# Performance work log

Hardware: AMD Instinct MI355X
Metric: run time of the kernel (lower is better)

The kernel has to match this reference:

```python
import jax, jax.numpy as jnp
import numpy as np

B, V, J, NB = 512, 6890, 24, 10
P = (J - 1) * 9  # 207 pose-blendshape features
# Standard SMPL kinematic tree (parents[0] = -1 for root)
PARENTS = np.array([-1, 0, 0, 0, 1, 2, 3, 4, 5, 6, 7, 8, 9, 9, 9, 12, 13, 14, 16, 17, 18, 19, 20, 21])


def rodrigues(aa):
    """Axis-angle [N,3] -> rotation matrices [N,3,3] (batch_rodrigues)."""
    angle = jnp.linalg.norm(aa, axis=-1, keepdims=True) + 1e-8
    axis = aa / angle
    x, y, z = axis[..., 0], axis[..., 1], axis[..., 2]
    zero = jnp.zeros_like(x)
    K = jnp.stack([zero, -z, y, z, zero, -x, -y, x, zero], axis=-1).reshape(aa.shape[0], 3, 3)
    s = jnp.sin(angle)[..., None]
    c = jnp.cos(angle)[..., None]
    return jnp.eye(3, dtype=aa.dtype) + s * K + (1.0 - c) * jnp.matmul(K, K)


def setup_inputs() -> dict:
    key = jax.random.key(0)
    ks = jax.random.split(key, 9)
    J_reg = jax.random.uniform(ks[7], (J, V), dtype=jnp.float32)
    J_reg = J_reg / jnp.sum(J_reg, axis=1, keepdims=True)
    W = jax.nn.softmax(4.0 * jax.random.normal(ks[8], (V, J), dtype=jnp.float32), axis=-1)
    return {
        "betas": jax.random.normal(ks[0], (B, NB), dtype=jnp.float32),
        "body_pose": 0.3 * jax.random.normal(ks[1], (B, (J - 1) * 3), dtype=jnp.float32),
        "global_orient": 0.3 * jax.random.normal(ks[2], (B, 3), dtype=jnp.float32),
        "transl": jax.random.normal(ks[3], (B, 3), dtype=jnp.float32),
        "v_template": jax.random.normal(ks[4], (V, 3), dtype=jnp.float32),
        "shapedirs": 0.01 * jax.random.normal(ks[5], (V, 3, NB), dtype=jnp.float32),
        "posedirs": 0.01 * jax.random.normal(ks[6], (P, V * 3), dtype=jnp.float32),
        "J_regressor": J_reg,
        "lbs_weights": W,
    }


def reference(betas, body_pose, global_orient, transl, v_template, shapedirs, posedirs, J_regressor, lbs_weights):
    b = betas.shape[0]
    # --- pose to rotation matrices (pose2rot=True path) ---
    full_pose = jnp.concatenate([global_orient, body_pose], axis=-1)  # [B, 72]
    rot_mats = rodrigues(full_pose.reshape(-1, 3)).reshape(b, J, 3, 3)
    # --- shape blend shapes ---
    v_shaped = v_template + jnp.einsum('bl,vcl->bvc', betas, shapedirs)  # [B,V,3]
    joints = jnp.einsum('jv,bvc->bjc', J_regressor, v_shaped)            # [B,J,3]
    # --- pose blend shapes ---
    pose_feature = (rot_mats[:, 1:] - jnp.eye(3, dtype=rot_mats.dtype)).reshape(b, P)
    v_posed = v_shaped + (pose_feature @ posedirs).reshape(b, V, 3)
    # --- kinematic chain (batch_rigid_transform) ---
    rel_joints = joints.at[:, 1:].add(-joints[:, PARENTS[1:]])
    top = jnp.concatenate([rot_mats, rel_joints[..., None]], axis=-1)   # [B,J,3,4]
    bottom = jnp.broadcast_to(jnp.array([0.0, 0.0, 0.0, 1.0], dtype=rot_mats.dtype), (b, J, 1, 4))
    mats = jnp.concatenate([top, bottom], axis=-2)                      # [B,J,4,4]
    chain = [mats[:, 0]]
    for i in range(1, J):  # fixed 24-joint serial composition
        chain.append(chain[PARENTS[i]] @ mats[:, i])
    A = jnp.stack(chain, axis=1)                                        # [B,J,4,4]
    posed_joints = A[..., :3, 3]
    # remove rest-pose joint locations from the transforms
    t_rel = A[..., :3, 3] - jnp.einsum('bjmn,bjn->bjm', A[..., :3, :3], joints)
    A_rel = A.at[..., :3, 3].set(t_rel)
    # --- linear blend skinning ---
    T = jnp.einsum('vj,bjmn->bvmn', lbs_weights, A_rel)                 # [B,V,4,4]
    verts = jnp.einsum('bvmn,bvn->bvm', T[..., :3, :3], v_posed) + T[..., :3, 3]
    vertices = verts + transl[:, None]
    joints_out = posed_joints + transl[:, None]
    return vertices, joints_out
```

## Files before the change

kernel.cpp:

```cpp
#include <hip/hip_runtime.h>
#include <hip/hip_bf16.h>
#include <math.h>

#define Bn 512
#define Vn 6890
#define NBn 10
#define Pn 207
#define N3n 20670
#define KP 224
#define VPAD 6912

typedef __attribute__((ext_vector_type(8))) short short8v;
typedef __attribute__((ext_vector_type(4))) float f32x4;

__constant__ int c_par[24] = {-1,0,0,0,1,2,3,4,5,6,7,8,9,9,9,12,13,14,16,17,18,19,20,21};
__constant__ int c_lvl[10] = {0,1,4,7,10,15,18,20,22,24};

static __device__ __forceinline__ unsigned short f2bf(float f) {
  union { float f; unsigned u; } x; x.f = f;
  unsigned r = x.u + 0x7FFFu + ((x.u >> 16) & 1u);
  return (unsigned short)(r >> 16);
}
static __device__ __forceinline__ float bf2f(unsigned short h) {
  union { unsigned u; float f; } x; x.u = ((unsigned)h) << 16; return x.f;
}


__global__ __launch_bounds__(256) void k_prep(
    const float* __restrict__ Jreg, const float* __restrict__ vtpl,
    const float* __restrict__ sdirs, const float* __restrict__ pdirs,
    const float* __restrict__ W, float* __restrict__ part,
    unsigned short* __restrict__ B_lin,
    unsigned short* __restrict__ W_hi, unsigned short* __restrict__ W_lo)
{
  const int tid = threadIdx.x;
  if (blockIdx.x < 576) {
    const int bid = blockIdx.x % 72;
    const int chunk = blockIdx.x / 72;
    const int j = bid / 3, c = bid % 3;
    const int vlo = chunk * 862;
    const int vhi = min(Vn, vlo + 862);
    float acc[11];
#pragma unroll
    for (int k = 0; k < 11; k++) acc[k] = 0.f;
    for (int v = vlo + tid; v < vhi; v += 256) {
      float w = Jreg[(size_t)j * Vn + v];
      int n = v * 3 + c;
#pragma unroll
      for (int l = 0; l < 10; l++) acc[l] += w * sdirs[(size_t)n * 10 + l];
      acc[10] += w * vtpl[n];
    }
    __shared__ float red[256];
    for (int k = 0; k < 11; k++) {
      red[tid] = acc[k];
      __syncthreads();
      for (int s = 128; s > 0; s >>= 1) {
        if (tid < s) red[tid] += red[tid + s];
        __syncthreads();
      }
      if (tid == 0) part[(size_t)chunk * 792 + bid * 11 + k] = red[0];
      __syncthreads();
    }
  } else if (blockIdx.x < 576 + 2268) {
    const int pair = (blockIdx.x - 576) * 4 + (tid >> 6);
    const int l = tid & 63;
    const int nt = pair / 7, s = pair % 7;
    const int col = nt * 16 + (l & 15);
    const int kb = s * 32 + ((l >> 4) << 3);
    unsigned short vals[8];
#pragma unroll
    for (int j = 0; j < 8; j++) {
      int k = kb + j;
      unsigned short u = 0;
      if (col < N3n) {
        if (k < Pn) u = f2bf(pdirs[(size_t)k * N3n + col]);
        else if (k < 217) u = f2bf(sdirs[(size_t)col * 10 + (k - 207)]);
        else if (k == 217) u = f2bf(vtpl[col]);
        else if (k == 218) {
          float t = vtpl[col];
          u = f2bf(t - bf2f(f2bf(t)));
        }
      }
      vals[j] = u;
    }
    uint4 o;
    o.x = (unsigned)vals[0] | ((unsigned)vals[1] << 16);
    o.y = (unsigned)vals[2] | ((unsigned)vals[3] << 16);
    o.z = (unsigned)vals[4] | ((unsigned)vals[5] << 16);
    o.w = (unsigned)vals[6] | ((unsigned)vals[7] << 16);
    *(uint4*)(B_lin + (size_t)pair * 512 + l * 8) = o;
  } else {
    int idx = (blockIdx.x - 576 - 2268) * 256 + tid;
    if (idx < VPAD * 32) {
      int v = idx >> 5, k = idx & 31;
      float f = (v < Vn && k < 24) ? W[(size_t)v * 24 + k] : 0.f;
      unsigned short hi = f2bf(f);
      W_hi[idx] = hi;
      W_lo[idx] = f2bf(f - bf2f(hi));
    }
  }
}

__global__ __launch_bounds__(64) void k_pose2(
    const float* __restrict__ betas, const float* __restrict__ body_pose,
    const float* __restrict__ gorient, const float* __restrict__ transl,
    const float* __restrict__ part,
    unsigned short* __restrict__ pf_bf,
    unsigned short* __restrict__ Ar_hi, unsigned short* __restrict__ Ar_lo,
    float* __restrict__ out_joints)
{
  const int b = blockIdx.x;
  const int tid = threadIdx.x;
  __shared__ float JS_s[720];
  __shared__ float Jt_s[72];
  __shared__ float Rs[24][9];
  __shared__ float jnt[24][3];
  __shared__ float rel[24][3];
  __shared__ float A_s[24][12];

  for (int idx = tid; idx < 792; idx += 64) {
    float s = 0.f;
#pragma unroll
    for (int y = 0; y < 8; y++) s += part[(size_t)y * 792 + idx];
    int bid = idx / 11, k = idx % 11;
    if (k < 10) JS_s[bid * 10 + k] = s;
    else        Jt_s[bid] = s;
  }

  if (tid < 24) {
    float x, y, z;
    if (tid == 0) { x = gorient[b*3+0]; y = gorient[b*3+1]; z = gorient[b*3+2]; }
    else { int o = b*69 + (tid-1)*3; x = body_pose[o]; y = body_pose[o+1]; z = body_pose[o+2]; }
    float ang = sqrtf(x*x + y*y + z*z) + 1e-8f;
    float inv = 1.0f / ang;
    float ux = x*inv, uy = y*inv, uz = z*inv;
    float s = sinf(ang), cc = cosf(ang), omc = 1.0f - cc;
    float K[9] = {0.f, -uz, uy,  uz, 0.f, -ux,  -uy, ux, 0.f};
#pragma unroll
    for (int mm = 0; mm < 3; mm++)
#pragma unroll
      for (int nn = 0; nn < 3; nn++) {
        float kk = K[mm*3+0]*K[0+nn] + K[mm*3+1]*K[3+nn] + K[mm*3+2]*K[6+nn];
        float eye = (mm == nn) ? 1.0f : 0.0f;
        Rs[tid][mm*3+nn] = eye + s*K[mm*3+nn] + omc*kk;
      }
  }
  __syncthreads();

  for (int idx = tid; idx < 72; idx += 64) {
    float a = Jt_s[idx];
#pragma unroll
    for (int l = 0; l < 10; l++) a += betas[b*10 + l] * JS_s[idx*10 + l];
    jnt[idx/3][idx%3] = a;
  }
  for (int idx = tid; idx < KP; idx += 64) {
    unsigned short u = 0;
    if (idx < Pn) {
      int j = 1 + idx / 9, e = idx % 9;
      float eye = (e == 0 || e == 4 || e == 8) ? 1.0f : 0.0f;
      u = f2bf(Rs[j][e] - eye);
    } else if (idx < 217) {
      u = f2bf(betas[b*10 + (idx - 207)]);
    } else if (idx < 219) {
      u = 0x3F80;
    }
    pf_bf[(size_t)b * KP + idx] = u;
  }
  __syncthreads();
  for (int idx = tid; idx < 72; idx += 64) {
    int j = idx/3, cc = idx%3;
    float r = jnt[j][cc];
    if (j > 0) r -= jnt[c_par[j]][cc];
    rel[j][cc] = r;
  }
  __syncthreads();
  if (tid < 12) {
    int m = tid/4, nn = tid%4;
    A_s[0][tid] = (nn < 3) ? Rs[0][m*3+nn] : rel[0][m];
  }
  __syncthreads();
  for (int lev = 1; lev <= 8; lev++) {
    const int s0 = c_lvl[lev], s1 = c_lvl[lev + 1];
    const int jj = tid / 12, r = tid % 12;
    if (jj < s1 - s0) {
      const int i = s0 + jj;
      const int p = c_par[i];
      const int m = r >> 2, nn = r & 3;
      float v;
      if (nn < 3)
        v = A_s[p][m*4+0]*Rs[i][0+nn] + A_s[p][m*4+1]*Rs[i][3+nn] + A_s[p][m*4+2]*Rs[i][6+nn];
      else
        v = A_s[p][m*4+0]*rel[i][0] + A_s[p][m*4+1]*rel[i][1] + A_s[p][m*4+2]*rel[i][2] + A_s[p][m*4+3];
      A_s[i][r] = v;
    }
    __syncthreads();
  }
  for (int idx = tid; idx < 72; idx += 64) {
    int j = idx/3, cc = idx%3;
    out_joints[(size_t)b * 72 + idx] = A_s[j][cc*4+3] + transl[b*3+cc];
  }
  for (int idx = tid; idx < 512; idx += 64) {
    int e = idx >> 5, k = idx & 31;
    float a = 0.f;
    if (e < 12 && k < 24) {
      int m = e >> 2, nn = e & 3;
      if (nn < 3) a = A_s[k][m*4+nn];
      else a = A_s[k][m*4+3] - (A_s[k][m*4+0]*jnt[k][0] + A_s[k][m*4+1]*jnt[k][1] + A_s[k][m*4+2]*jnt[k][2]);
    }
    unsigned short hi = f2bf(a);
    Ar_hi[(size_t)b * 512 + idx] = hi;
    Ar_lo[(size_t)b * 512 + idx] = f2bf(a - bf2f(hi));
  }
}

__global__ __launch_bounds__(256) void k_mm2(
    const float* __restrict__ transl,
    const unsigned short* __restrict__ pf_bf, const unsigned short* __restrict__ B_lin,
    const unsigned short* __restrict__ W_hi, const unsigned short* __restrict__ W_lo,
    const unsigned short* __restrict__ Ar_hi, const unsigned short* __restrict__ Ar_lo,
    float* __restrict__ out)
{
  const int tid = threadIdx.x;
  const int l = tid & 63;
  const int wave = tid >> 6;
  const int b0 = blockIdx.x * 32;
  const int v0 = blockIdx.y * 64;

  __shared__ __align__(16) float vp[32][196];
  __shared__ float transl_s[32][3];

  if (tid < 96) transl_s[tid / 3][tid % 3] = transl[(size_t)b0 * 3 + tid];

  const unsigned short* pfb0 = pf_bf + (size_t)(b0 + (l & 15)) * KP + ((l >> 4) << 3);
  const unsigned short* pfb1 = pfb0 + 16 * KP;
  const int ntb = blockIdx.y * 12 + wave * 3;
  f32x4 a00 = {0.f,0.f,0.f,0.f}, a01 = a00, a02 = a00, a10 = a00, a11 = a00, a12 = a00;
#pragma unroll
  for (int s = 0; s < 7; s++) {
    short8v fa0 = *(const short8v*)(pfb0 + s * 32);
    short8v fa1 = *(const short8v*)(pfb1 + s * 32);
    short8v bv0 = *(const short8v*)(B_lin + ((size_t)(ntb + 0) * 7 + s) * 512 + l * 8);
    short8v bv1 = *(const short8v*)(B_lin + ((size_t)(ntb + 1) * 7 + s) * 512 + l * 8);
    short8v bv2 = *(const short8v*)(B_lin + ((size_t)(ntb + 2) * 7 + s) * 512 + l * 8);
    a00 = __builtin_amdgcn_mfma_f32_16x16x32_bf16(fa0, bv0, a00, 0, 0, 0);
    a01 = __builtin_amdgcn_mfma_f32_16x16x32_bf16(fa0, bv1, a01, 0, 0, 0);
    a02 = __builtin_amdgcn_mfma_f32_16x16x32_bf16(fa0, bv2, a02, 0, 0, 0);
    a10 = __builtin_amdgcn_mfma_f32_16x16x32_bf16(fa1, bv0, a10, 0, 0, 0);
    a11 = __builtin_amdgcn_mfma_f32_16x16x32_bf16(fa1, bv1, a11, 0, 0, 0);
    a12 = __builtin_amdgcn_mfma_f32_16x16x32_bf16(fa1, bv2, a12, 0, 0, 0);
  }
  {
    const int colb = wave * 48 + (l & 15);
    const int rowb = (l >> 4) * 4;
#pragma unroll
    for (int r = 0; r < 4; r++) {
      vp[rowb + r][colb]           = a00[r];
      vp[rowb + r][colb + 16]      = a01[r];
      vp[rowb + r][colb + 32]      = a02[r];
      vp[16 + rowb + r][colb]      = a10[r];
      vp[16 + rowb + r][colb + 16] = a11[r];
      vp[16 + rowb + r][colb + 32] = a12[r];
    }
  }
  __syncthreads();

  const int c = l & 15;
  const int g = l >> 4;
  const int kk = g << 3;

  short8v whi[4], wlo[4];
#pragma unroll
  for (int mt = 0; mt < 4; mt++) {
    const size_t wb = (size_t)(v0 + mt * 16 + c) * 32 + kk;
    whi[mt] = *(const short8v*)(W_hi + wb);
    wlo[mt] = *(const short8v*)(W_lo + wb);
  }

#pragma unroll
  for (int i = 0; i < 8; i++) {
    const int bl = wave * 8 + i;
    const size_t ab = (size_t)(b0 + bl) * 512 + c * 32 + kk;
    short8v ahi = *(const short8v*)(Ar_hi + ab);
    short8v alo = *(const short8v*)(Ar_lo + ab);
    const float trg = transl_s[bl][g < 3 ? g : 0];
#pragma unroll
    for (int mt = 0; mt < 4; mt++) {
      f32x4 t = {0.f, 0.f, 0.f, 0.f};
      t = __builtin_amdgcn_mfma_f32_16x16x32_bf16(alo, whi[mt], t, 0, 0, 0);
      t = __builtin_amdgcn_mfma_f32_16x16x32_bf16(ahi, wlo[mt], t, 0, 0, 0);
      t = __builtin_amdgcn_mfma_f32_16x16x32_bf16(ahi, whi[mt], t, 0, 0, 0);
      const int vl2 = mt * 16 + c;
      const int v = v0 + vl2;
      if (g < 3 && v < Vn) {
        float x = vp[bl][3 * vl2 + 0];
        float y = vp[bl][3 * vl2 + 1];
        float z = vp[bl][3 * vl2 + 2];
        out[((size_t)(b0 + bl) * Vn + v) * 3 + g] = t[0]*x + t[1]*y + t[2]*z + t[3] + trg;
      }
    }
  }
}


__global__ __launch_bounds__(256) void k_jsjt_part(
    const float* __restrict__ Jreg, const float* __restrict__ vtpl,
    const float* __restrict__ sdirs, float* __restrict__ part)
{
  const int bid = blockIdx.x;
  const int chunk = blockIdx.y;
  const int j = bid / 3, c = bid % 3;
  const int tid = threadIdx.x;
  const int vlo = chunk * 862;
  const int vhi = min(Vn, vlo + 862);
  float acc[11];
#pragma unroll
  for (int k = 0; k < 11; k++) acc[k] = 0.f;
  for (int v = vlo + tid; v < vhi; v += 256) {
    float w = Jreg[(size_t)j * Vn + v];
    int n = v * 3 + c;
#pragma unroll
    for (int l = 0; l < 10; l++) acc[l] += w * sdirs[(size_t)n * 10 + l];
    acc[10] += w * vtpl[n];
  }
  __shared__ float red[256];
  for (int k = 0; k < 11; k++) {
    red[tid] = acc[k];
    __syncthreads();
    for (int s = 128; s > 0; s >>= 1) {
      if (tid < s) red[tid] += red[tid + s];
      __syncthreads();
    }
    if (tid == 0) part[(size_t)chunk * 792 + bid * 11 + k] = red[0];
    __syncthreads();
  }
}

__global__ __launch_bounds__(1024) void k_jsjt_red(
    const float* __restrict__ part, float* __restrict__ JS, float* __restrict__ Jt)
{
  const int t = threadIdx.x;
  if (t >= 792) return;
  float s = 0.f;
#pragma unroll
  for (int y = 0; y < 8; y++) s += part[(size_t)y * 792 + t];
  int bid = t / 11, k = t % 11;
  if (k < 10) JS[bid * 10 + k] = s;
  else        Jt[bid] = s;
}

__global__ __launch_bounds__(64) void k_pose_fb(
    const float* __restrict__ betas, const float* __restrict__ body_pose,
    const float* __restrict__ gorient, const float* __restrict__ transl,
    const float* __restrict__ JS, const float* __restrict__ Jt,
    float* __restrict__ pf_ws, float* __restrict__ Ar_ws,
    float* __restrict__ out_joints)
{
  const int b = blockIdx.x;
  const int tid = threadIdx.x;
  __shared__ float Rs[24][9];
  __shared__ float jnt[24][3];
  __shared__ float rel[24][3];
  __shared__ float A_s[24][12];

  if (tid < 24) {
    float x, y, z;
    if (tid == 0) { x = gorient[b*3+0]; y = gorient[b*3+1]; z = gorient[b*3+2]; }
    else { int o = b*69 + (tid-1)*3; x = body_pose[o]; y = body_pose[o+1]; z = body_pose[o+2]; }
    float ang = sqrtf(x*x + y*y + z*z) + 1e-8f;
    float inv = 1.0f / ang;
    float ux = x*inv, uy = y*inv, uz = z*inv;
    float s = sinf(ang), cc = cosf(ang), omc = 1.0f - cc;
    float K[9] = {0.f, -uz, uy,  uz, 0.f, -ux,  -uy, ux, 0.f};
#pragma unroll
    for (int mm = 0; mm < 3; mm++)
#pragma unroll
      for (int nn = 0; nn < 3; nn++) {
        float kk = K[mm*3+0]*K[0+nn] + K[mm*3+1]*K[3+nn] + K[mm*3+2]*K[6+nn];
        float eye = (mm == nn) ? 1.0f : 0.0f;
        Rs[tid][mm*3+nn] = eye + s*K[mm*3+nn] + omc*kk;
      }
  }
  for (int idx = tid; idx < 72; idx += 64) {
    float a = Jt[idx];
#pragma unroll
    for (int l = 0; l < 10; l++) a += betas[b*10 + l] * JS[idx*10 + l];
    jnt[idx/3][idx%3] = a;
  }
  __syncthreads();
  for (int idx = tid; idx < Pn; idx += 64) {
    int j = 1 + idx / 9, e = idx % 9;
    float eye = (e == 0 || e == 4 || e == 8) ? 1.0f : 0.0f;
    pf_ws[(size_t)b * Pn + idx] = Rs[j][e] - eye;
  }
  for (int idx = tid; idx < 72; idx += 64) {
    int j = idx/3, cc = idx%3;
    float r = jnt[j][cc];
    if (j > 0) r -= jnt[c_par[j]][cc];
    rel[j][cc] = r;
  }
  __syncthreads();
  if (tid < 12) {
    int m = tid/4, nn = tid%4;
    A_s[0][tid] = (nn < 3) ? Rs[0][m*3+nn] : rel[0][m];
  }
  __syncthreads();
  for (int i = 1; i < 24; i++) {
    if (tid < 12) {
      int m = tid/4, nn = tid%4;
      int p = c_par[i];
      float v;
      if (nn < 3)
        v = A_s[p][m*4+0]*Rs[i][0+nn] + A_s[p][m*4+1]*Rs[i][3+nn] + A_s[p][m*4+2]*Rs[i][6+nn];
      else
        v = A_s[p][m*4+0]*rel[i][0] + A_s[p][m*4+1]*rel[i][1] + A_s[p][m*4+2]*rel[i][2] + A_s[p][m*4+3];
      A_s[i][tid] = v;
    }
    __syncthreads();
  }
  for (int idx = tid; idx < 72; idx += 64) {
    int j = idx/3, cc = idx%3;
    out_joints[(size_t)b * 72 + idx] = A_s[j][cc*4+3] + transl[b*3+cc];
  }
  for (int idx = tid; idx < 288; idx += 64) {
    int j = idx/12, r = idx%12, m = r/4, nn = r%4;
    float v;
    if (nn < 3) v = A_s[j][m*4+nn];
    else v = A_s[j][m*4+3] - (A_s[j][m*4+0]*jnt[j][0] + A_s[j][m*4+1]*jnt[j][1] + A_s[j][m*4+2]*jnt[j][2]);
    Ar_ws[(size_t)b * 288 + idx] = v;
  }
}

__global__ __launch_bounds__(192) void k_verts_fb(
    const float* __restrict__ betas, const float* __restrict__ transl,
    const float* __restrict__ vtpl, const float* __restrict__ sdirs,
    const float* __restrict__ pdirs, const float* __restrict__ W,
    const float* __restrict__ pf_ws, const float* __restrict__ Ar_ws,
    float* __restrict__ out)
{
  const int tid = threadIdx.x;
  const int b0 = blockIdx.x * 16;
  const int v0 = blockIdx.y * 128;
  const int n0 = v0 * 3;
  __shared__ __align__(16) float pf_s[Pn][16];
  __shared__ __align__(16) float Ar_s[16][288];
  __shared__ __align__(16) float vp_s[16][384];
  __shared__ float betas_s[16][NBn];
  __shared__ float transl_s[16][3];
  for (int idx = tid; idx < Pn * 16; idx += 192) {
    int p = idx >> 4, bi = idx & 15;
    pf_s[p][bi] = pf_ws[(size_t)(b0 + bi) * Pn + p];
  }
  for (int idx = tid; idx < 16 * 288; idx += 192)
    Ar_s[idx / 288][idx % 288] = Ar_ws[(size_t)b0 * 288 + idx];
  for (int idx = tid; idx < 16 * NBn; idx += 192)
    betas_s[idx / NBn][idx % NBn] = betas[(size_t)b0 * NBn + idx];
  for (int idx = tid; idx < 48; idx += 192)
    transl_s[idx / 3][idx % 3] = transl[(size_t)b0 * 3 + idx];
  __syncthreads();
  const int n = n0 + 2 * tid;
  const bool valid = (n < N3n);
  float acc0[16], acc1[16];
#pragma unroll
  for (int i = 0; i < 16; i++) { acc0[i] = 0.f; acc1[i] = 0.f; }
  for (int p = 0; p < Pn; p++) {
    float pd0 = 0.f, pd1 = 0.f;
    if (valid) { float2 t = *(const float2*)(pdirs + (size_t)p * N3n + n); pd0 = t.x; pd1 = t.y; }
    const float4* row = (const float4*)(pf_s[p]);
#pragma unroll
    for (int q = 0; q < 4; q++) {
      float4 f = row[q];
      acc0[4*q+0] += f.x * pd0;  acc1[4*q+0] += f.x * pd1;
      acc0[4*q+1] += f.y * pd0;  acc1[4*q+1] += f.y * pd1;
      acc0[4*q+2] += f.z * pd0;  acc1[4*q+2] += f.z * pd1;
      acc0[4*q+3] += f.w * pd0;  acc1[4*q+3] += f.w * pd1;
    }
  }
  float sd0[10], sd1[10], vt0 = 0.f, vt1 = 0.f;
#pragma unroll
  for (int l = 0; l < 10; l++) { sd0[l] = 0.f; sd1[l] = 0.f; }
  if (valid) {
    for (int l = 0; l < 10; l++) { sd0[l] = sdirs[(size_t)n*10 + l]; sd1[l] = sdirs[(size_t)n*10 + 10 + l]; }
    vt0 = vtpl[n]; vt1 = vtpl[n+1];
  }
#pragma unroll
  for (int bi = 0; bi < 16; bi++) {
    float s0 = vt0, s1 = vt1;
#pragma unroll
    for (int l = 0; l < 10; l++) { float bb = betas_s[bi][l]; s0 += bb*sd0[l]; s1 += bb*sd1[l]; }
    acc0[bi] += s0; acc1[bi] += s1;
  }
#pragma unroll
  for (int bi = 0; bi < 16; bi++) { vp_s[bi][2*tid] = acc0[bi]; vp_s[bi][2*tid+1] = acc1[bi]; }
  __syncthreads();
  const int m = tid / 64;
  const int vl = tid % 64;
  const int va = v0 + vl, vb = v0 + vl + 64;
  const bool va_ok = (va < Vn), vb_ok = (vb < Vn);
  float Wr0[24], Wr1[24];
#pragma unroll
  for (int j = 0; j < 24; j++) { Wr0[j] = 0.f; Wr1[j] = 0.f; }
  if (va_ok) { const float4* wp = (const float4*)(W + (size_t)va*24);
#pragma unroll
    for (int q = 0; q < 6; q++) { float4 f = wp[q]; Wr0[4*q]=f.x; Wr0[4*q+1]=f.y; Wr0[4*q+2]=f.z; Wr0[4*q+3]=f.w; } }
  if (vb_ok) { const float4* wp = (const float4*)(W + (size_t)vb*24);
#pragma unroll
    for (int q = 0; q < 6; q++) { float4 f = wp[q]; Wr1[4*q]=f.x; Wr1[4*q+1]=f.y; Wr1[4*q+2]=f.z; Wr1[4*q+3]=f.w; } }
  for (int bi = 0; bi < 16; bi++) {
    float Ta0=0.f,Ta1=0.f,Ta2=0.f,Ta3=0.f, Tb0=0.f,Tb1=0.f,Tb2=0.f,Tb3=0.f;
    const float4* arb = (const float4*)(Ar_s[bi]);
#pragma unroll
    for (int j = 0; j < 24; j++) {
      float4 a = arb[j*3 + m];
      float wa = Wr0[j], wb = Wr1[j];
      Ta0 += wa*a.x; Ta1 += wa*a.y; Ta2 += wa*a.z; Ta3 += wa*a.w;
      Tb0 += wb*a.x; Tb1 += wb*a.y; Tb2 += wb*a.z; Tb3 += wb*a.w;
    }
    float tr = transl_s[bi][m];
    if (va_ok) {
      float x = vp_s[bi][vl*3+0], y = vp_s[bi][vl*3+1], z = vp_s[bi][vl*3+2];
      out[((size_t)(b0+bi)*Vn + va)*3 + m] = Ta0*x + Ta1*y + Ta2*z + Ta3 + tr;
    }
    if (vb_ok) {
      float x = vp_s[bi][(vl+64)*3+0], y = vp_s[bi][(vl+64)*3+1], z = vp_s[bi][(vl+64)*3+2];
      out[((size_t)(b0+bi)*Vn + vb)*3 + m] = Tb0*x + Tb1*y + Tb2*z + Tb3 + tr;
    }
  }
}

extern "C" void kernel_launch(void* const* d_in, const int* in_sizes, int n_in,
                              void* d_out, int out_size, void* d_ws, size_t ws_size,
                              hipStream_t stream)
{
  const float *betas=nullptr, *bpose=nullptr, *gorient=nullptr, *transl=nullptr,
              *vtpl=nullptr, *sdirs=nullptr, *pdirs=nullptr, *Jreg=nullptr, *W=nullptr;
  int seen1536 = 0, seen165360 = 0;
  for (int i = 0; i < n_in; i++) {
    const float* p = (const float*)d_in[i];
    switch (in_sizes[i]) {
      case 5120:    betas = p; break;
      case 35328:   bpose = p; break;
      case 20670:   vtpl  = p; break;
      case 206700:  sdirs = p; break;
      case 4278690: pdirs = p; break;
      case 1536:    if (seen1536++ == 0) gorient = p; else transl = p; break;
      case 165360:  if (seen165360++ == 0) Jreg = p; else W = p; break;
      default: break;
    }
  }
  float* out = (float*)d_out;

  float* ws   = (float*)d_ws;
  float* part = ws;
  float* JS   = ws + 6336;
  float* Jt   = ws + 7056;
  float* pf   = ws + 7128;
  float* Ar   = ws + 113112;
  unsigned short* pf_bf = (unsigned short*)(ws + 260568);
  unsigned short* B_lin = (unsigned short*)(ws + 317912);
  unsigned short* W_hi  = (unsigned short*)(ws + 2640344);
  unsigned short* W_lo  = (unsigned short*)(ws + 2750936);
  unsigned short* Ar_hi = (unsigned short*)(ws + 2861528);
  unsigned short* Ar_lo = (unsigned short*)(ws + 2992600);
  const size_t WS_NEED = (size_t)3123672 * 4;
  const bool big = (ws_size >= WS_NEED);

  if (big) {
    k_prep<<<3708, 256, 0, stream>>>(Jreg, vtpl, sdirs, pdirs, W,
                                     part, B_lin, W_hi, W_lo);
    k_pose2<<<Bn, 64, 0, stream>>>(betas, bpose, gorient, transl, part,
                                   pf_bf, Ar_hi, Ar_lo,
                                   out + (size_t)Bn * Vn * 3);
    k_mm2<<<dim3(16, 108), 256, 0, stream>>>(transl, pf_bf, B_lin,
                                             W_hi, W_lo, Ar_hi, Ar_lo, out);
  } else {
    k_jsjt_part<<<dim3(72, 8), 256, 0, stream>>>(Jreg, vtpl, sdirs, part);
    k_jsjt_red<<<1, 1024, 0, stream>>>(part, JS, Jt);
    k_pose_fb<<<Bn, 64, 0, stream>>>(betas, bpose, gorient, transl, JS, Jt, pf, Ar,
                                     out + (size_t)Bn * Vn * 3);
    k_verts_fb<<<dim3(32, 54), 192, 0, stream>>>(betas, transl, vtpl, sdirs,
                                                 pdirs, W, pf, Ar, out);
  }
}
```

Measured before the change: 63.28 us.

## Switch MFMA paths to fp16, drop hi/lo splits, enlarge tiles, batch pose blocks

Moves the pose-blendshape and skinning matmuls from bf16 to fp16 MFMA. The skinning stage drops the three-term hi/lo split and uses a single fp16 product, and W and A_rel are stored once instead of twice. The main kernel now tiles 64 batches instead of 32 per block, and its grid is linearised and swizzled across vertex tiles for locality. The pose kernel packs 8 batch elements into one 512-thread block. Single fp16 skinning weights and transforms lose accuracy relative to the split scheme and risk exceeding tolerance, and the larger tile raises shared-memory and register use.

```diff
diff --git a/kernel.cpp b/kernel.cpp
--- a/kernel.cpp
+++ b/kernel.cpp
@@ -10,28 +10,18 @@
 #define KP 224
 #define VPAD 6912
 
-typedef __attribute__((ext_vector_type(8))) short short8v;
+typedef __attribute__((ext_vector_type(8))) _Float16 half8;
 typedef __attribute__((ext_vector_type(4))) float f32x4;
 
 __constant__ int c_par[24] = {-1,0,0,0,1,2,3,4,5,6,7,8,9,9,9,12,13,14,16,17,18,19,20,21};
 __constant__ int c_lvl[10] = {0,1,4,7,10,15,18,20,22,24};
-
-static __device__ __forceinline__ unsigned short f2bf(float f) {
-  union { float f; unsigned u; } x; x.f = f;
-  unsigned r = x.u + 0x7FFFu + ((x.u >> 16) & 1u);
-  return (unsigned short)(r >> 16);
-}
-static __device__ __forceinline__ float bf2f(unsigned short h) {
-  union { unsigned u; float f; } x; x.u = ((unsigned)h) << 16; return x.f;
-}
 
 
 __global__ __launch_bounds__(256) void k_prep(
     const float* __restrict__ Jreg, const float* __restrict__ vtpl,
     const float* __restrict__ sdirs, const float* __restrict__ pdirs,
     const float* __restrict__ W, float* __restrict__ part,
-    unsigned short* __restrict__ B_lin,
-    unsigned short* __restrict__ W_hi, unsigned short* __restrict__ W_lo)
+    _Float16* __restrict__ B_h, _Float16* __restrict__ W_h)
 {
   const int tid = threadIdx.x;
   if (blockIdx.x < 576) {
@@ -67,58 +57,53 @@
     const int nt = pair / 7, s = pair % 7;
     const int col = nt * 16 + (l & 15);
     const int kb = s * 32 + ((l >> 4) << 3);
-    unsigned short vals[8];
+    half8 hv;
 #pragma unroll
     for (int j = 0; j < 8; j++) {
       int k = kb + j;
-      unsigned short u = 0;
+      float f = 0.f;
       if (col < N3n) {
-        if (k < Pn) u = f2bf(pdirs[(size_t)k * N3n + col]);
-        else if (k < 217) u = f2bf(sdirs[(size_t)col * 10 + (k - 207)]);
-        else if (k == 217) u = f2bf(vtpl[col]);
+        if (k < Pn) f = pdirs[(size_t)k * N3n + col];
+        else if (k < 217) f = sdirs[(size_t)col * 10 + (k - 207)];
+        else if (k == 217) f = (float)(_Float16)vtpl[col];
         else if (k == 218) {
           float t = vtpl[col];
-          u = f2bf(t - bf2f(f2bf(t)));
+          f = t - (float)(_Float16)t;
         }
       }
-      vals[j] = u;
-    }
-    uint4 o;
-    o.x = (unsigned)vals[0] | ((unsigned)vals[1] << 16);
-    o.y = (unsigned)vals[2] | ((unsigned)vals[3] << 16);
-    o.z = (unsigned)vals[4] | ((unsigned)vals[5] << 16);
-    o.w = (unsigned)vals[6] | ((unsigned)vals[7] << 16);
-    *(uint4*)(B_lin + (size_t)pair * 512 + l * 8) = o;
+      hv[j] = (_Float16)f;
+    }
+    *(half8*)(B_h + (size_t)pair * 512 + l * 8) = hv;
   } else {
     int idx = (blockIdx.x - 576 - 2268) * 256 + tid;
     if (idx < VPAD * 32) {
       int v = idx >> 5, k = idx & 31;
       float f = (v < Vn && k < 24) ? W[(size_t)v * 24 + k] : 0.f;
-      unsigned short hi = f2bf(f);
-      W_hi[idx] = hi;
-      W_lo[idx] = f2bf(f - bf2f(hi));
-    }
-  }
-}
-
-__global__ __launch_bounds__(64) void k_pose2(
+      W_h[idx] = (_Float16)f;
+    }
+  }
+}
+
+__global__ __launch_bounds__(512) void k_pose2(
     const float* __restrict__ betas, const float* __restrict__ body_pose,
     const float* __restrict__ gorient, const float* __restrict__ transl,
     const float* __restrict__ part,
-    unsigned short* __restrict__ pf_bf,
-    unsigned short* __restrict__ Ar_hi, unsigned short* __restrict__ Ar_lo,
+    _Float16* __restrict__ pf_h, _Float16* __restrict__ Ar_h,
     float* __restrict__ out_joints)
 {
-  const int b = blockIdx.x;
   const int tid = threadIdx.x;
+  const int wave = tid >> 6;
+  const int lane = tid & 63;
+  const int b = blockIdx.x * 8 + wave;
+
   __shared__ float JS_s[720];
   __shared__ float Jt_s[72];
-  __shared__ float Rs[24][9];
-  __shared__ float jnt[24][3];
-  __shared__ float rel[24][3];
-  __shared__ float A_s[24][12];
-
-  for (int idx = tid; idx < 792; idx += 64) {
+  __shared__ float Rs[8][24][9];
+  __shared__ float jnt[8][24][3];
+  __shared__ float rel[8][24][3];
+  __shared__ float A_s[8][24][12];
+
+  for (int idx = tid; idx < 792; idx += 512) {
     float s = 0.f;
 #pragma unroll
     for (int y = 0; y < 8; y++) s += part[(size_t)y * 792 + idx];
@@ -127,10 +112,10 @@
     else        Jt_s[bid] = s;
   }
 
-  if (tid < 24) {
+  if (lane < 24) {
     float x, y, z;
-    if (tid == 0) { x = gorient[b*3+0]; y = gorient[b*3+1]; z = gorient[b*3+2]; }
-    else { int o = b*69 + (tid-1)*3; x = body_pose[o]; y = body_pose[o+1]; z = body_pose[o+2]; }
+    if (lane == 0) { x = gorient[b*3+0]; y = gorient[b*3+1]; z = gorient[b*3+2]; }
+    else { int o = b*69 + (lane-1)*3; x = body_pose[o]; y = body_pose[o+1]; z = body_pose[o+2]; }
     float ang = sqrtf(x*x + y*y + z*z) + 1e-8f;
     float inv = 1.0f / ang;
     float ux = x*inv, uy = y*inv, uz = z*inv;
@@ -142,125 +127,133 @@
       for (int nn = 0; nn < 3; nn++) {
         float kk = K[mm*3+0]*K[0+nn] + K[mm*3+1]*K[3+nn] + K[mm*3+2]*K[6+nn];
         float eye = (mm == nn) ? 1.0f : 0.0f;
-        Rs[tid][mm*3+nn] = eye + s*K[mm*3+nn] + omc*kk;
+        Rs[wave][lane][mm*3+nn] = eye + s*K[mm*3+nn] + omc*kk;
       }
   }
   __syncthreads();
 
-  for (int idx = tid; idx < 72; idx += 64) {
+  for (int idx = lane; idx < 72; idx += 64) {
     float a = Jt_s[idx];
 #pragma unroll
     for (int l = 0; l < 10; l++) a += betas[b*10 + l] * JS_s[idx*10 + l];
-    jnt[idx/3][idx%3] = a;
-  }
-  for (int idx = tid; idx < KP; idx += 64) {
-    unsigned short u = 0;
+    jnt[wave][idx/3][idx%3] = a;
+  }
+  for (int idx = lane; idx < KP; idx += 64) {
+    float f = 0.f;
     if (idx < Pn) {
       int j = 1 + idx / 9, e = idx % 9;
       float eye = (e == 0 || e == 4 || e == 8) ? 1.0f : 0.0f;
-      u = f2bf(Rs[j][e] - eye);
+      f = Rs[wave][j][e] - eye;
     } else if (idx < 217) {
-      u = f2bf(betas[b*10 + (idx - 207)]);
+      f = betas[b*10 + (idx - 207)];
     } else if (idx < 219) {
-      u = 0x3F80;
-    }
-    pf_bf[(size_t)b * KP + idx] = u;
-  }
-  __syncthreads();
-  for (int idx = tid; idx < 72; idx += 64) {
+      f = 1.0f;
+    }
+    pf_h[(size_t)b * KP + idx] = (_Float16)f;
+  }
+  __syncthreads();
+  for (int idx = lane; idx < 72; idx += 64) {
     int j = idx/3, cc = idx%3;
-    float r = jnt[j][cc];
-    if (j > 0) r -= jnt[c_par[j]][cc];
-    rel[j][cc] = r;
-  }
-  __syncthreads();
-  if (tid < 12) {
-    int m = tid/4, nn = tid%4;
-    A_s[0][tid] = (nn < 3) ? Rs[0][m*3+nn] : rel[0][m];
+    float r = jnt[wave][j][cc];
+    if (j > 0) r -= jnt[wave][c_par[j]][cc];
+    rel[wave][j][cc] = r;
+  }
+  __syncthreads();
+  if (lane < 12) {
+    int m = lane/4, nn = lane%4;
+    A_s[wave][0][lane] = (nn < 3) ? Rs[wave][0][m*3+nn] : rel[wave][0][m];
   }
   __syncthreads();
   for (int lev = 1; lev <= 8; lev++) {
     const int s0 = c_lvl[lev], s1 = c_lvl[lev + 1];
-    const int jj = tid / 12, r = tid % 12;
+    const int jj = lane / 12, r = lane % 12;
     if (jj < s1 - s0) {
       const int i = s0 + jj;
       const int p = c_par[i];
       const int m = r >> 2, nn = r & 3;
       float v;
       if (nn < 3)
-        v = A_s[p][m*4+0]*Rs[i][0+nn] + A_s[p][m*4+1]*Rs[i][3+nn] + A_s[p][m*4+2]*Rs[i][6+nn];
+        v = A_s[wave][p][m*4+0]*Rs[wave][i][0+nn] + A_s[wave][p][m*4+1]*Rs[wave][i][3+nn] + A_s[wave][p][m*4+2]*Rs[wave][i][6+nn];
       else
-        v = A_s[p][m*4+0]*rel[i][0] + A_s[p][m*4+1]*rel[i][1] + A_s[p][m*4+2]*rel[i][2] + A_s[p][m*4+3];
-      A_s[i][r] = v;
+        v = A_s[wave][p][m*4+0]*rel[wave][i][0] + A_s[wave][p][m*4+1]*rel[wave][i][1] + A_s[wave][p][m*4+2]*rel[wave][i][2] + A_s[wave][p][m*4+3];
+      A_s[wave][i][r] = v;
     }
     __syncthreads();
   }
-  for (int idx = tid; idx < 72; idx += 64) {
+  for (int idx = lane; idx < 72; idx += 64) {
     int j = idx/3, cc = idx%3;
-    out_joints[(size_t)b * 72 + idx] = A_s[j][cc*4+3] + transl[b*3+cc];
-  }
-  for (int idx = tid; idx < 512; idx += 64) {
+    out_joints[(size_t)b * 72 + idx] = A_s[wave][j][cc*4+3] + transl[b*3+cc];
+  }
+  for (int idx = lane; idx < 512; idx += 64) {
     int e = idx >> 5, k = idx & 31;
     float a = 0.f;
     if (e < 12 && k < 24) {
       int m = e >> 2, nn = e & 3;
-      if (nn < 3) a = A_s[k][m*4+nn];
-      else a = A_s[k][m*4+3] - (A_s[k][m*4+0]*jnt[k][0] + A_s[k][m*4+1]*jnt[k][1] + A_s[k][m*4+2]*jnt[k][2]);
-    }
-    unsigned short hi = f2bf(a);
-    Ar_hi[(size_t)b * 512 + idx] = hi;
-    Ar_lo[(size_t)b * 512 + idx] = f2bf(a - bf2f(hi));
-  }
-}
-
-__global__ __launch_bounds__(256) void k_mm2(
+      if (nn < 3) a = A_s[wave][k][m*4+nn];
+      else a = A_s[wave][k][m*4+3] - (A_s[wave][k][m*4+0]*jnt[wave][k][0] + A_s[wave][k][m*4+1]*jnt[wave][k][1] + A_s[wave][k][m*4+2]*jnt[wave][k][2]);
+    }
+    Ar_h[(size_t)b * 512 + idx] = (_Float16)a;
+  }
+}
+
+__global__ __launch_bounds__(256) void k_mm3(
     const float* __restrict__ transl,
-    const unsigned short* __restrict__ pf_bf, const unsigned short* __restrict__ B_lin,
-    const unsigned short* __restrict__ W_hi, const unsigned short* __restrict__ W_lo,
-    const unsigned short* __restrict__ Ar_hi, const unsigned short* __restrict__ Ar_lo,
+    const _Float16* __restrict__ pf_h, const _Float16* __restrict__ B_h,
+    const _Float16* __restrict__ W_h, const _Float16* __restrict__ Ar_h,
     float* __restrict__ out)
 {
+  const int lin = blockIdx.x;
+  const int r8 = lin & 7;
+  const int k2 = lin >> 3;
+  const int b_t = k2 & 7;
+  const int m8 = k2 >> 3;
+  const int v_t = r8 * 14 + m8;
+  if (v_t >= 108) return;
+
   const int tid = threadIdx.x;
   const int l = tid & 63;
   const int wave = tid >> 6;
-  const int b0 = blockIdx.x * 32;
-  const int v0 = blockIdx.y * 64;
-
-  __shared__ __align__(16) float vp[32][196];
-  __shared__ float transl_s[32][3];
-
-  if (tid < 96) transl_s[tid / 3][tid % 3] = transl[(size_t)b0 * 3 + tid];
-
-  const unsigned short* pfb0 = pf_bf + (size_t)(b0 + (l & 15)) * KP + ((l >> 4) << 3);
-  const unsigned short* pfb1 = pfb0 + 16 * KP;
-  const int ntb = blockIdx.y * 12 + wave * 3;
-  f32x4 a00 = {0.f,0.f,0.f,0.f}, a01 = a00, a02 = a00, a10 = a00, a11 = a00, a12 = a00;
+  const int b0 = b_t * 64;
+  const int v0 = v_t * 64;
+
+  __shared__ __align__(16) float vp[64][196];
+  __shared__ float transl_s[64][3];
+
+  if (tid < 192) transl_s[tid / 3][tid % 3] = transl[(size_t)b0 * 3 + tid];
+
+  const int c0 = l & 15;
+  const int kk0 = (l >> 4) << 3;
+  const int ntb = v_t * 12 + wave * 3;
+  f32x4 acc[4][3];
+#pragma unroll
+  for (int t = 0; t < 4; t++)
+#pragma unroll
+    for (int n = 0; n < 3; n++) acc[t][n] = (f32x4){0.f, 0.f, 0.f, 0.f};
+
 #pragma unroll
   for (int s = 0; s < 7; s++) {
-    short8v fa0 = *(const short8v*)(pfb0 + s * 32);
-    short8v fa1 = *(const short8v*)(pfb1 + s * 32);
-    short8v bv0 = *(const short8v*)(B_lin + ((size_t)(ntb + 0) * 7 + s) * 512 + l * 8);
-    short8v bv1 = *(const short8v*)(B_lin + ((size_t)(ntb + 1) * 7 + s) * 512 + l * 8);
-    short8v bv2 = *(const short8v*)(B_lin + ((size_t)(ntb + 2) * 7 + s) * 512 + l * 8);
-    a00 = __builtin_amdgcn_mfma_f32_16x16x32_bf16(fa0, bv0, a00, 0, 0, 0);
-    a01 = __builtin_amdgcn_mfma_f32_16x16x32_bf16(fa0, bv1, a01, 0, 0, 0);
-    a02 = __builtin_amdgcn_mfma_f32_16x16x32_bf16(fa0, bv2, a02, 0, 0, 0);
-    a10 = __builtin_amdgcn_mfma_f32_16x16x32_bf16(fa1, bv0, a10, 0, 0, 0);
-    a11 = __builtin_amdgcn_mfma_f32_16x16x32_bf16(fa1, bv1, a11, 0, 0, 0);
-    a12 = __builtin_amdgcn_mfma_f32_16x16x32_bf16(fa1, bv2, a12, 0, 0, 0);
+    half8 bv[3];
+#pragma unroll
+    for (int n = 0; n < 3; n++)
+      bv[n] = *(const half8*)(B_h + ((size_t)(ntb + n) * 7 + s) * 512 + l * 8);
+#pragma unroll
+    for (int t = 0; t < 4; t++) {
+      half8 fa = *(const half8*)(pf_h + (size_t)(b0 + t * 16 + c0) * KP + kk0 + s * 32);
+#pragma unroll
+      for (int n = 0; n < 3; n++)
+        acc[t][n] = __builtin_amdgcn_mfma_f32_16x16x32_f16(fa, bv[n], acc[t][n], 0, 0, 0);
+    }
   }
   {
-    const int colb = wave * 48 + (l & 15);
+    const int colb = wave * 48 + c0;
     const int rowb = (l >> 4) * 4;
 #pragma unroll
-    for (int r = 0; r < 4; r++) {
-      vp[rowb + r][colb]           = a00[r];
-      vp[rowb + r][colb + 16]      = a01[r];
-      vp[rowb + r][colb + 32]      = a02[r];
-      vp[16 + rowb + r][colb]      = a10[r];
-      vp[16 + rowb + r][colb + 16] = a11[r];
-      vp[16 + rowb + r][colb + 32] = a12[r];
-    }
+    for (int t = 0; t < 4; t++)
+#pragma unroll
+      for (int n = 0; n < 3; n++)
+#pragma unroll
+        for (int r = 0; r < 4; r++)
+          vp[t * 16 + rowb + r][colb + n * 16] = acc[t][n][r];
   }
   __syncthreads();
 
@@ -268,27 +261,20 @@
   const int g = l >> 4;
   const int kk = g << 3;
 
-  short8v whi[4], wlo[4];
-#pragma unroll
-  for (int mt = 0; mt < 4; mt++) {
-    const size_t wb = (size_t)(v0 + mt * 16 + c) * 32 + kk;
-    whi[mt] = *(const short8v*)(W_hi + wb);
-    wlo[mt] = *(const short8v*)(W_lo + wb);
-  }
-
-#pragma unroll
-  for (int i = 0; i < 8; i++) {
-    const int bl = wave * 8 + i;
-    const size_t ab = (size_t)(b0 + bl) * 512 + c * 32 + kk;
-    short8v ahi = *(const short8v*)(Ar_hi + ab);
-    short8v alo = *(const short8v*)(Ar_lo + ab);
+  half8 wh[4];
+#pragma unroll
+  for (int mt = 0; mt < 4; mt++)
+    wh[mt] = *(const half8*)(W_h + (size_t)(v0 + mt * 16 + c) * 32 + kk);
+
+#pragma unroll
+  for (int i = 0; i < 16; i++) {
+    const int bl = wave * 16 + i;
+    half8 ah = *(const half8*)(Ar_h + (size_t)(b0 + bl) * 512 + c * 32 + kk);
     const float trg = transl_s[bl][g < 3 ? g : 0];
 #pragma unroll
     for (int mt = 0; mt < 4; mt++) {
       f32x4 t = {0.f, 0.f, 0.f, 0.f};
-      t = __builtin_amdgcn_mfma_f32_16x16x32_bf16(alo, whi[mt], t, 0, 0, 0);
-      t = __builtin_amdgcn_mfma_f32_16x16x32_bf16(ahi, wlo[mt], t, 0, 0, 0);
-      t = __builtin_amdgcn_mfma_f32_16x16x32_bf16(ahi, whi[mt], t, 0, 0, 0);
+      t = __builtin_amdgcn_mfma_f32_16x16x32_f16(ah, wh[mt], t, 0, 0, 0);
       const int vl2 = mt * 16 + c;
       const int v = v0 + vl2;
       if (g < 3 && v < Vn) {
@@ -555,23 +541,18 @@
   float* Jt   = ws + 7056;
   float* pf   = ws + 7128;
   float* Ar   = ws + 113112;
-  unsigned short* pf_bf = (unsigned short*)(ws + 260568);
-  unsigned short* B_lin = (unsigned short*)(ws + 317912);
-  unsigned short* W_hi  = (unsigned short*)(ws + 2640344);
-  unsigned short* W_lo  = (unsigned short*)(ws + 2750936);
-  unsigned short* Ar_hi = (unsigned short*)(ws + 2861528);
-  unsigned short* Ar_lo = (unsigned short*)(ws + 2992600);
+  _Float16* pf_h = (_Float16*)(ws + 260568);
+  _Float16* B_h  = (_Float16*)(ws + 317912);
+  _Float16* W_h  = (_Float16*)(ws + 2640344);
+  _Float16* Ar_h = (_Float16*)(ws + 2861528);
   const size_t WS_NEED = (size_t)3123672 * 4;
   const bool big = (ws_size >= WS_NEED);
 
   if (big) {
-    k_prep<<<3708, 256, 0, stream>>>(Jreg, vtpl, sdirs, pdirs, W,
-                                     part, B_lin, W_hi, W_lo);
-    k_pose2<<<Bn, 64, 0, stream>>>(betas, bpose, gorient, transl, part,
-                                   pf_bf, Ar_hi, Ar_lo,
-                                   out + (size_t)Bn * Vn * 3);
-    k_mm2<<<dim3(16, 108), 256, 0, stream>>>(transl, pf_bf, B_lin,
-                                             W_hi, W_lo, Ar_hi, Ar_lo, out);
+    k_prep<<<3708, 256, 0, stream>>>(Jreg, vtpl, sdirs, pdirs, W, part, B_h, W_h);
+    k_pose2<<<64, 512, 0, stream>>>(betas, bpose, gorient, transl, part,
+                                    pf_h, Ar_h, out + (size_t)Bn * Vn * 3);
+    k_mm3<<<896, 256, 0, stream>>>(transl, pf_h, B_h, W_h, Ar_h, out);
   } else {
     k_jsjt_part<<<dim3(72, 8), 256, 0, stream>>>(Jreg, vtpl, sdirs, part);
     k_jsjt_red<<<1, 1024, 0, stream>>>(part, JS, Jt);
```

Result: faster. 59.89 us (-5.4%).
